# Kernel tuning notes

Hardware: AMD Instinct MI355X
Metric: run time of the kernel (lower is better)

## Reference

```python
import jax, jax.numpy as jnp
import numpy as np

N, CIN, T, V = 64, 192, 256, 25
K, COUT, S = 3, 64, 5  # kernel_size, out_channels, num_semantic


def setup_inputs() -> dict:
    key = jax.random.key(0)
    ks = jax.random.split(key, 8)
    x = jax.random.normal(ks[0], (N, CIN, T, V), jnp.float32)
    A = jax.random.normal(ks[1], (K, V, V), jnp.float32)
    node_type = jnp.arange(V, dtype=jnp.int64) % S  # every semantic type present
    Wc = jax.random.normal(ks[2], (COUT * K, CIN), jnp.float32) * 0.02
    bc = jax.random.normal(ks[3], (COUT * K,), jnp.float32) * 0.02
    W1 = jax.random.normal(ks[4], (S * COUT, COUT * K), jnp.float32) * 0.02
    b1 = jax.random.normal(ks[5], (S * COUT,), jnp.float32) * 0.02
    W2 = jax.random.normal(ks[6], (S * COUT, COUT * K), jnp.float32) * 0.02
    b2 = jax.random.normal(ks[7], (S * COUT,), jnp.float32) * 0.02
    return {"x": x, "A": A, "node_type": node_type, "Wc": Wc, "bc": bc,
            "W1": W1, "b1": b1, "W2": W2, "b2": b2}


def reference(x, A, node_type, Wc, bc, W1, b1, W2, b2):
    # self.conv: 1x1 conv (t_kernel_size=1) -> (N, K*COUT, T, V)
    y = jnp.einsum('nctv,oc->notv', x, Wc) + bc[None, :, None, None]
    # conv1 / conv2 applied to tmp_x = y, reshape to (N, S, COUT, T, V), mean over T
    x1 = (jnp.einsum('nctv,oc->notv', y, W1) + b1[None, :, None, None]).reshape(N, S, COUT, T, V)
    x2 = (jnp.einsum('nctv,oc->notv', y, W2) + b2[None, :, None, None]).reshape(N, S, COUT, T, V)
    x1 = x1.mean(axis=3, keepdims=True)  # (N, S, COUT, 1, V)
    x2 = x2.mean(axis=3, keepdims=True)  # (N, S, COUT, 1, V)
    # per-semantic masked mean over nodes (vectorized over the 5 semantic types)
    masks = (node_type[None, :] == jnp.arange(S)[:, None]).astype(y.dtype)  # (S, V)
    counts = masks.sum(axis=-1)  # (S,)
    sem = jnp.einsum('nsclv,sv->nscl', x1, masks) / counts[None, :, None, None]  # (N,S,COUT,1)
    # diff: (N, S, COUT, 1, 1, V)  (graph_list stacked over the semantic axis)
    graphs = sem[..., None, None] - x2[:, :, :, :, None, :]
    # graph conv with adjacency A
    xk = y.reshape(N, K, COUT, T, V)
    out = jnp.einsum('nkctv,kvw->nctw', xk, A)  # (N, COUT, T, V)
    return out, A, graphs
```

## Files before the change

### kernel.cpp

```cpp
#include <hip/hip_runtime.h>

#define N_    64
#define CIN_  192
#define T_    256
#define V_    25
#define K_    3
#define COUT_ 64
#define OC_   192
#define SS_   5

#define OUT_OFF_A (N_*COUT_*T_*V_)
#define OUT_OFF_G (OUT_OFF_A + K_*V_*V_)

#define TCH   4
#define HCH   4
#define NCOLS 100
#define XB_STRIDE 200
#define YB_STRIDE 104
#define UNION_SHORTS 26624
#define NYV  4800
#define CPN  (T_/(TCH*HCH))
#define NBLK (N_*CPN)
#define CHUNK_UNITS ((CIN_/8)*NCOLS)

typedef __attribute__((ext_vector_type(8))) short short8;
typedef __attribute__((ext_vector_type(4))) float float4v;

__device__ inline unsigned bf16r(float f) {
    unsigned u = __float_as_uint(f);
    return (u + 0x7fffu + ((u >> 16) & 1u)) >> 16;
}

__global__ __launch_bounds__(256) void prep(const float* __restrict__ Wc,
                                            const float* __restrict__ A,
                                            short* __restrict__ WcB,
                                            short* __restrict__ A2T,
                                            float* __restrict__ out) {
    int idx = blockIdx.x * 256 + threadIdx.x;
    if (idx < OC_ * CIN_) WcB[idx] = (short)bf16r(Wc[idx]);
    if (idx < 32 * YB_STRIDE) {
        int w = idx / YB_STRIDE, kk = idx - w * YB_STRIDE;
        short val = 0;
        if (w < V_ && kk < K_ * V_) {
            int k = kk / V_, v = kk - k * V_;
            val = (short)bf16r(A[k * V_ * V_ + v * V_ + w]);
        }
        A2T[idx] = val;
    }
    if (idx < K_ * V_ * V_) out[OUT_OFF_A + idx] = A[idx];
}

__global__ __launch_bounds__(256, 2) void fused_mfma(const float* __restrict__ x,
                                                     const short* __restrict__ WcB,
                                                     const float* __restrict__ bc,
                                                     const short* __restrict__ A2T,
                                                     float* __restrict__ out,
                                                     float* __restrict__ part) {
    __shared__ __align__(16) short U[UNION_SHORTS];

    const int tid  = threadIdx.x;
    const int lane = tid & 63;
    const int wv   = tid >> 6;
    const int l15  = lane & 15;
    const int q    = lane >> 4;
    const int n    = blockIdx.x >> 4;
    const int tc   = blockIdx.x & 15;

    {
        int4 z = make_int4(0, 0, 0, 0);
        for (int i = tid; i < UNION_SHORTS / 8; i += 256) ((int4*)U)[i] = z;
    }

    short8 wfrag[3][6];
    const int rt0 = wv * 3;
    {
        const short* wb = WcB + (rt0 * 16 + l15) * CIN_ + q * 8;
#pragma unroll
        for (int j = 0; j < 3; ++j)
#pragma unroll
            for (int ks = 0; ks < 6; ++ks)
                wfrag[j][ks] = *(const short8*)(wb + j * 16 * CIN_ + ks * 32);
    }

    float racc[19];
#pragma unroll
    for (int u = 0; u < 19; ++u) racc[u] = 0.f;

    for (int h = 0; h < HCH; ++h) {
        const int t0 = tc * (TCH * HCH) + h * TCH;
        __syncthreads();

        const float* xn = x + (size_t)n * (CIN_ * T_ * V_) + t0 * V_;
        for (int u = tid; u < CHUNK_UNITS; u += 256) {
            int col = u % NCOLS;
            int cg  = u / NCOLS;
            const float* xp = xn + (size_t)cg * 8 * (T_ * V_) + col;
            short8 s;
#pragma unroll
            for (int j = 0; j < 8; ++j)
                s[j] = (short)bf16r(xp[(size_t)j * (T_ * V_)]);
            *(short8*)&U[col * XB_STRIDE + cg * 8] = s;
        }
        __syncthreads();

        float4v acc[3][7];
        {
            float4v bvec[3];
#pragma unroll
            for (int j = 0; j < 3; ++j)
                bvec[j] = *(const float4v*)(bc + (rt0 + j) * 16 + q * 4);
#pragma unroll
            for (int j = 0; j < 3; ++j)
#pragma unroll
                for (int ct = 0; ct < 7; ++ct) acc[j][ct] = bvec[j];
        }

#pragma unroll
        for (int ct = 0; ct < 7; ++ct) {
            const short* xb = &U[(ct * 16 + l15) * XB_STRIDE + q * 8];
#pragma unroll
            for (int ks = 0; ks < 6; ++ks) {
                short8 bfrag = *(const short8*)(xb + ks * 32);
#pragma unroll
                for (int j = 0; j < 3; ++j)
                    acc[j][ct] = __builtin_amdgcn_mfma_f32_16x16x32_bf16(
                        wfrag[j][ks], bfrag, acc[j][ct], 0, 0, 0);
            }
        }
        __syncthreads();

#pragma unroll
        for (int ct = 0; ct < 7; ++ct) {
            int col = ct * 16 + l15;
            if (col < NCOLS) {
                int tl = col / V_;
                int v  = col - tl * V_;
#pragma unroll
                for (int j = 0; j < 3; ++j) {
                    int obase = (rt0 + j) * 16 + q * 4;
#pragma unroll
                    for (int i = 0; i < 4; ++i) {
                        int o   = obase + i;
                        int row = tl * 64 + (o & 63);
                        int cY  = (o >> 6) * V_ + v;
                        U[row * YB_STRIDE + cY] = (short)bf16r(acc[j][ct][i]);
                    }
                }
            }
        }
        __syncthreads();

        short8 b2[2][3];
#pragma unroll
        for (int nt = 0; nt < 2; ++nt)
#pragma unroll
            for (int ks = 0; ks < 3; ++ks)
                b2[nt][ks] = *(const short8*)&A2T[(nt * 16 + l15) * YB_STRIDE + ks * 32 + q * 8];

        float4v o2[4][2];
#pragma unroll
        for (int mt = 0; mt < 4; ++mt)
#pragma unroll
            for (int nt = 0; nt < 2; ++nt) o2[mt][nt] = (float4v){0.f, 0.f, 0.f, 0.f};

#pragma unroll
        for (int mt = 0; mt < 4; ++mt) {
            int m = (wv * 4 + mt) * 16 + l15;
            const short* yb = &U[m * YB_STRIDE + q * 8];
#pragma unroll
            for (int ks = 0; ks < 3; ++ks) {
                short8 af = *(const short8*)(yb + ks * 32);
#pragma unroll
                for (int nt = 0; nt < 2; ++nt)
                    o2[mt][nt] = __builtin_amdgcn_mfma_f32_16x16x32_bf16(
                        af, b2[nt][ks], o2[mt][nt], 0, 0, 0);
            }
        }

#pragma unroll
        for (int mt = 0; mt < 4; ++mt) {
#pragma unroll
            for (int nt = 0; nt < 2; ++nt) {
                int w = nt * 16 + l15;
                if (w < V_) {
#pragma unroll
                    for (int i = 0; i < 4; ++i) {
                        int m  = (wv * 4 + mt) * 16 + q * 4 + i;
                        int cc = m & 63, tl = m >> 6;
                        out[((size_t)(n * COUT_ + cc) * T_ + (t0 + tl)) * V_ + w] = o2[mt][nt][i];
                    }
                }
            }
        }

#pragma unroll
        for (int u = 0; u < 19; ++u) {
            int idx = tid + u * 256;
            if (u < 18 || idx < NYV) {
                int o = idx / V_, v = idx - (idx / V_) * V_;
                int cc = o & 63, k = o >> 6;
                const short* yp = &U[cc * YB_STRIDE + k * V_ + v];
                float s = 0.f;
#pragma unroll
                for (int tl = 0; tl < TCH; ++tl) {
                    unsigned b = (unsigned short)yp[tl * 64 * YB_STRIDE];
                    s += __uint_as_float(b << 16);
                }
                racc[u] += s;
            }
        }
    }

    float* pb = part + (size_t)blockIdx.x * NYV;
#pragma unroll
    for (int u = 0; u < 19; ++u) {
        int idx = tid + u * 256;
        if (u < 18 || idx < NYV) pb[idx] = racc[u];
    }
}

__global__ __launch_bounds__(256) void yred(const float* __restrict__ part,
                                            float* __restrict__ ysum) {
    int i = blockIdx.x * 256 + threadIdx.x;
    if (i >= N_ * NYV) return;
    int n = i / NYV;
    int r = i - n * NYV;
    const float* p = part + (size_t)n * CPN * NYV + r;
    float s = 0.f;
#pragma unroll
    for (int tc = 0; tc < CPN; ++tc) s += p[tc * NYV];
    ysum[i] = s * (1.0f / T_);
}

__global__ __launch_bounds__(256) void e2_graphs(const float* __restrict__ ysum,
                                                 const float* __restrict__ W1,
                                                 const float* __restrict__ b1,
                                                 const float* __restrict__ W2,
                                                 const float* __restrict__ b2,
                                                 const int* __restrict__ node_type,
                                                 float* __restrict__ out) {
    __shared__ float s1[10][V_];
    __shared__ float sem[10];
    const int tid = threadIdx.x;
    const int n  = blockIdx.x >> 5;
    const int jc = blockIdx.x & 31;
    const int jl = tid / V_;
    const int v  = tid - jl * V_;
    const int j  = jc * 10 + jl;
    float x2 = 0.f;
    if (jl < 10) {
        const float* yb = ysum + (size_t)n * NYV + v;
        const float* w1 = W1 + j * OC_;
        const float* w2 = W2 + j * OC_;
        float a1 = b1[j], a2 = b2[j];
        for (int o = 0; o < OC_; ++o) {
            float yv = yb[o * V_];
            a1 += w1[o] * yv;
            a2 += w2[o] * yv;
        }
        s1[jl][v] = a1;
        x2 = a2;
    }
    __syncthreads();
    if (tid < 10) {
        int s = (jc * 10 + tid) >> 6;
        float sum = 0.f, cnt = 0.f;
        for (int vv = 0; vv < V_; ++vv)
            if (node_type[vv] == s) { sum += s1[tid][vv]; cnt += 1.f; }
        sem[tid] = sum / cnt;
    }
    __syncthreads();
    if (jl < 10)
        out[OUT_OFF_G + (size_t)n * (SS_ * COUT_ * V_) + j * V_ + v] = sem[jl] - x2;
}

extern "C" void kernel_launch(void* const* d_in, const int* in_sizes, int n_in,
                              void* d_out, int out_size, void* d_ws, size_t ws_size,
                              hipStream_t stream) {
    const float* x         = (const float*)d_in[0];
    const float* A         = (const float*)d_in[1];
    const int*   node_type = (const int*)d_in[2];
    const float* Wc        = (const float*)d_in[3];
    const float* bc        = (const float*)d_in[4];
    const float* W1        = (const float*)d_in[5];
    const float* b1        = (const float*)d_in[6];
    const float* W2        = (const float*)d_in[7];
    const float* b2        = (const float*)d_in[8];
    float* out = (float*)d_out;

    float* part = (float*)d_ws;
    float* ysum = part + (size_t)NBLK * NYV;
    short* WcB  = (short*)(ysum + N_ * NYV);
    short* A2T  = WcB + OC_ * CIN_;

    hipLaunchKernelGGL(prep, dim3((OC_ * CIN_ + 255) / 256), dim3(256), 0, stream,
                       Wc, A, WcB, A2T, out);
    hipLaunchKernelGGL(fused_mfma, dim3(NBLK), dim3(256), 0, stream,
                       x, WcB, bc, A2T, out, part);
    hipLaunchKernelGGL(yred, dim3((N_ * NYV + 255) / 256), dim3(256), 0, stream,
                       part, ysum);
    hipLaunchKernelGGL(e2_graphs, dim3(N_ * 32), dim3(256), 0, stream,
                       ysum, W1, b1, W2, b2, node_type, out);
}
```

Before: 637.5 us.

## Double-buffer x staging in LDS with register prefetch and smaller time chunks

```diff
diff --git a/kernel.cpp b/kernel.cpp
--- a/kernel.cpp
+++ b/kernel.cpp
@@ -12,16 +12,19 @@
 #define OUT_OFF_A (N_*COUT_*T_*V_)
 #define OUT_OFF_G (OUT_OFF_A + K_*V_*V_)
 
-#define TCH   4
-#define HCH   4
-#define NCOLS 100
+#define TCH   2
+#define HCH   8
+#define NCOLS 50
+#define NCT   4
 #define XB_STRIDE 200
 #define YB_STRIDE 104
-#define UNION_SHORTS 26624
+#define YB_ROWS 128
+#define BUF_SHORTS 13312
 #define NYV  4800
 #define CPN  (T_/(TCH*HCH))
 #define NBLK (N_*CPN)
 #define CHUNK_UNITS ((CIN_/8)*NCOLS)
+#define UPT 5
 
 typedef __attribute__((ext_vector_type(8))) short short8;
 typedef __attribute__((ext_vector_type(4))) float float4v;
@@ -50,13 +53,13 @@
     if (idx < K_ * V_ * V_) out[OUT_OFF_A + idx] = A[idx];
 }
 
-__global__ __launch_bounds__(256, 2) void fused_mfma(const float* __restrict__ x,
+__global__ __launch_bounds__(256, 3) void fused_mfma(const float* __restrict__ x,
                                                      const short* __restrict__ WcB,
                                                      const float* __restrict__ bc,
                                                      const short* __restrict__ A2T,
                                                      float* __restrict__ out,
                                                      float* __restrict__ part) {
-    __shared__ __align__(16) short U[UNION_SHORTS];
+    __shared__ __align__(16) short U[2 * BUF_SHORTS];
 
     const int tid  = threadIdx.x;
     const int lane = tid & 63;
@@ -65,72 +68,98 @@
     const int q    = lane >> 4;
     const int n    = blockIdx.x >> 4;
     const int tc   = blockIdx.x & 15;
+    const int rt0  = wv * 3;
 
     {
         int4 z = make_int4(0, 0, 0, 0);
-        for (int i = tid; i < UNION_SHORTS / 8; i += 256) ((int4*)U)[i] = z;
-    }
-
-    short8 wfrag[3][6];
-    const int rt0 = wv * 3;
+        for (int i = tid; i < 2 * BUF_SHORTS / 8; i += 256) ((int4*)U)[i] = z;
+    }
+    __syncthreads();
+
+    float4v bvec[3];
+#pragma unroll
+    for (int j = 0; j < 3; ++j)
+        bvec[j] = *(const float4v*)(bc + (rt0 + j) * 16 + q * 4);
+
+    float racc[19];
+#pragma unroll
+    for (int u = 0; u < 19; ++u) racc[u] = 0.f;
+
+    const float* xn = x + (size_t)n * (CIN_ * T_ * V_);
+    const int tbase = tc * (TCH * HCH);
+
     {
-        const short* wb = WcB + (rt0 * 16 + l15) * CIN_ + q * 8;
-#pragma unroll
-        for (int j = 0; j < 3; ++j)
-#pragma unroll
-            for (int ks = 0; ks < 6; ++ks)
-                wfrag[j][ks] = *(const short8*)(wb + j * 16 * CIN_ + ks * 32);
-    }
-
-    float racc[19];
-#pragma unroll
-    for (int u = 0; u < 19; ++u) racc[u] = 0.f;
-
-    for (int h = 0; h < HCH; ++h) {
-        const int t0 = tc * (TCH * HCH) + h * TCH;
-        __syncthreads();
-
-        const float* xn = x + (size_t)n * (CIN_ * T_ * V_) + t0 * V_;
+        const float* x0 = xn + (size_t)tbase * V_;
         for (int u = tid; u < CHUNK_UNITS; u += 256) {
-            int col = u % NCOLS;
-            int cg  = u / NCOLS;
-            const float* xp = xn + (size_t)cg * 8 * (T_ * V_) + col;
+            int col = u % NCOLS, cg = u / NCOLS;
+            const float* xp = x0 + (size_t)cg * 8 * (T_ * V_) + col;
             short8 s;
 #pragma unroll
             for (int j = 0; j < 8; ++j)
                 s[j] = (short)bf16r(xp[(size_t)j * (T_ * V_)]);
             *(short8*)&U[col * XB_STRIDE + cg * 8] = s;
         }
+    }
+
+    for (int h = 0; h < HCH; ++h) {
+        const int bs = (h & 1) * BUF_SHORTS;
+        const int ob = ((h & 1) ^ 1) * BUF_SHORTS;
+        const int t0 = tbase + h * TCH;
+        const bool stage_ok = (h < HCH - 1);
+
         __syncthreads();
 
-        float4v acc[3][7];
+        float4v acc[3][NCT];
+#pragma unroll
+        for (int j = 0; j < 3; ++j)
+#pragma unroll
+            for (int ct = 0; ct < NCT; ++ct) acc[j][ct] = bvec[j];
+
+        short8 wcur[6], wnxt[6];
         {
-            float4v bvec[3];
-#pragma unroll
-            for (int j = 0; j < 3; ++j)
-                bvec[j] = *(const float4v*)(bc + (rt0 + j) * 16 + q * 4);
-#pragma unroll
-            for (int j = 0; j < 3; ++j)
-#pragma unroll
-                for (int ct = 0; ct < 7; ++ct) acc[j][ct] = bvec[j];
-        }
-
-#pragma unroll
-        for (int ct = 0; ct < 7; ++ct) {
-            const short* xb = &U[(ct * 16 + l15) * XB_STRIDE + q * 8];
-#pragma unroll
-            for (int ks = 0; ks < 6; ++ks) {
-                short8 bfrag = *(const short8*)(xb + ks * 32);
-#pragma unroll
-                for (int j = 0; j < 3; ++j)
+            const short* wb = WcB + (rt0 * 16 + l15) * CIN_ + q * 8;
+#pragma unroll
+            for (int ks = 0; ks < 6; ++ks) wcur[ks] = *(const short8*)(wb + ks * 32);
+        }
+#pragma unroll
+        for (int j = 0; j < 3; ++j) {
+            if (j < 2) {
+                const short* wb = WcB + ((rt0 + j + 1) * 16 + l15) * CIN_ + q * 8;
+#pragma unroll
+                for (int ks = 0; ks < 6; ++ks) wnxt[ks] = *(const short8*)(wb + ks * 32);
+            }
+#pragma unroll
+            for (int ct = 0; ct < NCT; ++ct) {
+                const short* xb = &U[bs + (ct * 16 + l15) * XB_STRIDE + q * 8];
+#pragma unroll
+                for (int ks = 0; ks < 6; ++ks) {
+                    short8 bfrag = *(const short8*)(xb + ks * 32);
                     acc[j][ct] = __builtin_amdgcn_mfma_f32_16x16x32_bf16(
-                        wfrag[j][ks], bfrag, acc[j][ct], 0, 0, 0);
+                        wcur[ks], bfrag, acc[j][ct], 0, 0, 0);
+                }
+            }
+            if (j < 2) {
+#pragma unroll
+                for (int ks = 0; ks < 6; ++ks) wcur[ks] = wnxt[ks];
             }
         }
         __syncthreads();
 
-#pragma unroll
-        for (int ct = 0; ct < 7; ++ct) {
+        float tmp[UPT][8];
+        const float* x1 = xn + (size_t)(t0 + TCH) * V_;
+#pragma unroll
+        for (int s = 0; s < UPT; ++s) {
+            int u = tid + s * 256;
+            if (stage_ok && u < CHUNK_UNITS) {
+                int col = u % NCOLS, cg = u / NCOLS;
+                const float* xp = x1 + (size_t)cg * 8 * (T_ * V_) + col;
+#pragma unroll
+                for (int j = 0; j < 8; ++j) tmp[s][j] = xp[(size_t)j * (T_ * V_)];
+            }
+        }
+
+#pragma unroll
+        for (int ct = 0; ct < NCT; ++ct) {
             int col = ct * 16 + l15;
             if (col < NCOLS) {
                 int tl = col / V_;
@@ -143,7 +172,7 @@
                         int o   = obase + i;
                         int row = tl * 64 + (o & 63);
                         int cY  = (o >> 6) * V_ + v;
-                        U[row * YB_STRIDE + cY] = (short)bf16r(acc[j][ct][i]);
+                        U[bs + row * YB_STRIDE + cY] = (short)bf16r(acc[j][ct][i]);
                     }
                 }
             }
@@ -157,16 +186,16 @@
             for (int ks = 0; ks < 3; ++ks)
                 b2[nt][ks] = *(const short8*)&A2T[(nt * 16 + l15) * YB_STRIDE + ks * 32 + q * 8];
 
-        float4v o2[4][2];
-#pragma unroll
-        for (int mt = 0; mt < 4; ++mt)
+        float4v o2[2][2];
+#pragma unroll
+        for (int mt = 0; mt < 2; ++mt)
 #pragma unroll
             for (int nt = 0; nt < 2; ++nt) o2[mt][nt] = (float4v){0.f, 0.f, 0.f, 0.f};
 
 #pragma unroll
-        for (int mt = 0; mt < 4; ++mt) {
-            int m = (wv * 4 + mt) * 16 + l15;
-            const short* yb = &U[m * YB_STRIDE + q * 8];
+        for (int mt = 0; mt < 2; ++mt) {
+            int m = (wv * 2 + mt) * 16 + l15;
+            const short* yb = &U[bs + m * YB_STRIDE + q * 8];
 #pragma unroll
             for (int ks = 0; ks < 3; ++ks) {
                 short8 af = *(const short8*)(yb + ks * 32);
@@ -178,14 +207,14 @@
         }
 
 #pragma unroll
-        for (int mt = 0; mt < 4; ++mt) {
+        for (int mt = 0; mt < 2; ++mt) {
 #pragma unroll
             for (int nt = 0; nt < 2; ++nt) {
                 int w = nt * 16 + l15;
                 if (w < V_) {
 #pragma unroll
                     for (int i = 0; i < 4; ++i) {
-                        int m  = (wv * 4 + mt) * 16 + q * 4 + i;
+                        int m  = (wv * 2 + mt) * 16 + q * 4 + i;
                         int cc = m & 63, tl = m >> 6;
                         out[((size_t)(n * COUT_ + cc) * T_ + (t0 + tl)) * V_ + w] = o2[mt][nt][i];
                     }
@@ -199,7 +228,7 @@
             if (u < 18 || idx < NYV) {
                 int o = idx / V_, v = idx - (idx / V_) * V_;
                 int cc = o & 63, k = o >> 6;
-                const short* yp = &U[cc * YB_STRIDE + k * V_ + v];
+                const short* yp = &U[bs + cc * YB_STRIDE + k * V_ + v];
                 float s = 0.f;
 #pragma unroll
                 for (int tl = 0; tl < TCH; ++tl) {
@@ -207,6 +236,20 @@
                     s += __uint_as_float(b << 16);
                 }
                 racc[u] += s;
+            }
+        }
+
+        if (stage_ok) {
+#pragma unroll
+            for (int s = 0; s < UPT; ++s) {
+                int u = tid + s * 256;
+                if (u < CHUNK_UNITS) {
+                    int col = u % NCOLS, cg = u / NCOLS;
+                    short8 sv;
+#pragma unroll
+                    for (int j = 0; j < 8; ++j) sv[j] = (short)bf16r(tmp[s][j]);
+                    *(short8*)&U[ob + col * XB_STRIDE + cg * 8] = sv;
+                }
             }
         }
     }
```

After: 1.653 ms. 159% more time.
